# Performance work log

Measured on AMD Instinct MI355X. Metric: run time of the kernel, lower is better.

The kernel has to match this reference:

```python
import jax, jax.numpy as jnp
import numpy as np

NUM_HEADS = 32
HEAD_DIM = 128
NUM_KV_HEADS = 8
SCALE = 0.08838834764831845  # 1/sqrt(128)
SEQ_LEN = 2048
TOTAL_TOKENS = 4096  # batch=2 sequences of 2048


def setup_inputs() -> dict:
    key = jax.random.key(0)
    kq, kk, kv = jax.random.split(key, 3)
    q = jax.random.normal(kq, (TOTAL_TOKENS, NUM_HEADS * HEAD_DIM), dtype=jnp.float32)
    k = jax.random.normal(kk, (TOTAL_TOKENS, NUM_KV_HEADS * HEAD_DIM), dtype=jnp.float32)
    v = jax.random.normal(kv, (TOTAL_TOKENS, NUM_KV_HEADS * HEAD_DIM), dtype=jnp.float32)
    return {"q": q, "k": k, "v": v, "seq_len": SEQ_LEN}


def reference(q, k, v, seq_len):
    # Unified (varlen) causal GQA attention: flattened tokens are split into
    # batch sequences of equal length (the prefill path of the unified kernel).
    T = q.shape[0]
    B = T // seq_len
    G = NUM_HEADS // NUM_KV_HEADS  # query heads per kv head
    # [B, S, Hkv, G, D] and [B, S, Hkv, D]
    qh = q.reshape(B, seq_len, NUM_KV_HEADS, G, HEAD_DIM)
    kh = k.reshape(B, seq_len, NUM_KV_HEADS, HEAD_DIM)
    vh = v.reshape(B, seq_len, NUM_KV_HEADS, HEAD_DIM)
    # scores: [B, Hkv, G, Sq, Sk]
    scores = jnp.einsum("bqhgd,bkhd->bhgqk", qh, kh) * SCALE
    causal = jnp.tril(jnp.ones((seq_len, seq_len), dtype=bool))
    scores = jnp.where(causal, scores, jnp.finfo(scores.dtype).min)
    probs = jax.nn.softmax(scores, axis=-1)
    # out: [B, Sq, Hkv, G, D]
    o = jnp.einsum("bhgqk,bkhd->bqhgd", probs, vh)
    return o.reshape(T, NUM_HEADS * HEAD_DIM)
```

## Files before the change

### kernel.cpp

```cpp
#include <hip/hip_runtime.h>
#include <stdint.h>
#include <stddef.h>


#define S_LEN   2048
#define HQ      32
#define HKV     8
#define DH      128
#define QSTRIDE (HQ*DH)
#define KSTRIDE (HKV*DH)
#define SCALE_L2 0.12751139830213113f
#define DEFER_THR 8.0f

#define KTILE      64
#define NTILES     (S_LEN/KTILE)
#define CSTRIDE    520
#define KPART      (16*CSTRIDE)
#define TILE_ELEMS (KPART + 16*CSTRIDE)

typedef __bf16 bf16;
typedef short        s16x4 __attribute__((ext_vector_type(4)));
typedef short        s16x8 __attribute__((ext_vector_type(8)));
typedef float        f32x4 __attribute__((ext_vector_type(4)));
typedef unsigned int u32x2 __attribute__((ext_vector_type(2)));
typedef unsigned int u32x4 __attribute__((ext_vector_type(4)));

__device__ __forceinline__ unsigned int pk2(float a, float b) {
  union { bf16 h[2]; unsigned int u; } x;
  x.h[0] = (bf16)a; x.h[1] = (bf16)b;
  return x.u;
}

__device__ __forceinline__ int koff(int chunk, int key) {
  return chunk*CSTRIDE + key*8;
}
__device__ __forceinline__ int voff(int unit, int d) {
  return KPART + unit*CSTRIDE + d*4;
}

__global__ __launch_bounds__(512, 4)
void attn_fwd(const float* __restrict__ qg, const float* __restrict__ kg,
              const float* __restrict__ vg, float* __restrict__ og) {
  __shared__ bf16 smem[2*TILE_ELEMS];

  const int tid   = threadIdx.x;
  const int lane  = tid & 63;
  const int wave  = tid >> 6;
  const int l15   = lane & 15;
  const int quad  = lane >> 4;
  const int pairp = blockIdx.x;
  const int h     = blockIdx.y;
  const int b     = blockIdx.z;
  const int hkv   = h >> 2;

  const int fk_key = tid >> 3, fk_cg = tid & 7;
  const int fv_u   = tid & 15, fv_dq = tid >> 4;
  float4 fkx[4], fvx[4];

  auto load_regs = [&](int t) {
    const float* kp = kg + (size_t)(b*S_LEN + t*KTILE + fk_key)*KSTRIDE
                         + hkv*DH + fk_cg*16;
#pragma unroll
    for (int i = 0; i < 4; ++i) fkx[i] = ((const float4*)kp)[i];
    const int d0 = fv_dq*4;
#pragma unroll
    for (int j = 0; j < 4; ++j)
      fvx[j] = *(const float4*)(vg + (size_t)(b*S_LEN + t*KTILE + fv_u*4 + j)*KSTRIDE
                                   + hkv*DH + d0);
  };
  auto store_tile = [&](int bi) {
    bf16* kb = smem + bi*TILE_ELEMS;
#pragma unroll
    for (int ii = 0; ii < 2; ++ii) {
      u32x4 w;
      w[0] = pk2(fkx[2*ii].x,   fkx[2*ii].y);   w[1] = pk2(fkx[2*ii].z,   fkx[2*ii].w);
      w[2] = pk2(fkx[2*ii+1].x, fkx[2*ii+1].y); w[3] = pk2(fkx[2*ii+1].z, fkx[2*ii+1].w);
      *(u32x4*)(kb + koff(fk_cg*2 + ii, fk_key)) = w;
    }
    const float* g0 = (const float*)&fvx[0];
    const float* g1 = (const float*)&fvx[1];
    const float* g2 = (const float*)&fvx[2];
    const float* g3 = (const float*)&fvx[3];
#pragma unroll
    for (int i = 0; i < 4; i += 2) {
      u32x4 w;
      w[0] = pk2(g0[i],   g1[i]);
      w[1] = pk2(g2[i],   g3[i]);
      w[2] = pk2(g0[i+1], g1[i+1]);
      w[3] = pk2(g2[i+1], g3[i+1]);
      *(u32x4*)(kb + voff(fv_u, fv_dq*4 + i)) = w;
    }
  };

  f32x4 oacc[8];
  float m_run, l_run;
  u32x4 qf[4];

  const int qbs[2] = { pairp, 15 - pairp };
  load_regs(0);

  int gs = 0;
#pragma unroll 1
  for (int item = 0; item < 2; ++item) {
    const int qblk = qbs[item];
    const int qw   = qblk*128 + wave*16;
    const int nst  = qblk*2 + 2;

    {
      const float* qp = qg + (size_t)(b*S_LEN + qw + l15)*QSTRIDE
                           + h*DH + quad*8;
#pragma unroll
      for (int c = 0; c < 4; ++c) {
        const float4 a4 = ((const float4*)(qp + c*32))[0];
        const float4 b4 = ((const float4*)(qp + c*32))[1];
        u32x4 w;
        w[0] = pk2(a4.x*SCALE_L2, a4.y*SCALE_L2);
        w[1] = pk2(a4.z*SCALE_L2, a4.w*SCALE_L2);
        w[2] = pk2(b4.x*SCALE_L2, b4.y*SCALE_L2);
        w[3] = pk2(b4.z*SCALE_L2, b4.w*SCALE_L2);
        qf[c] = w;
      }
    }
#pragma unroll
    for (int nd = 0; nd < 8; ++nd) oacc[nd] = (f32x4){0.f, 0.f, 0.f, 0.f};
    m_run = -3e38f; l_run = 0.f;

#pragma unroll 1
    for (int i = 0; i < nst; ++i, ++gs) {
      const int k0  = i*KTILE;
      const int buf = gs & 1;
      store_tile(buf);
      const bool more  = (i + 1 < nst);
      const bool cross = (!more) && (item == 0);
      if (more)       load_regs(i + 1);
      else if (cross) load_regs(0);
      __syncthreads();

      if (k0 <= qw + 15) {
        const bf16* kb = smem + buf*TILE_ELEMS;

        f32x4 sacc[4];
#pragma unroll
        for (int mt = 0; mt < 4; ++mt) sacc[mt] = (f32x4){0.f, 0.f, 0.f, 0.f};
#pragma unroll
        for (int c = 0; c < 4; ++c) {
#pragma unroll
          for (int mt = 0; mt < 4; ++mt) {
            const u32x4 af = *(const u32x4*)(kb + koff(c*4 + quad, mt*16 + l15));
            sacc[mt] = __builtin_amdgcn_mfma_f32_16x16x32_bf16(
                __builtin_bit_cast(s16x8, af), __builtin_bit_cast(s16x8, qf[c]),
                sacc[mt], 0, 0, 0);
          }
        }

        const bool needmask = (k0 + KTILE - 1 > qw);
        const int  qgl = qw + l15;
        if (needmask) {
#pragma unroll
          for (int mt = 0; mt < 4; ++mt)
#pragma unroll
            for (int r = 0; r < 4; ++r) {
              const int key = k0 + mt*16 + quad*4 + r;
              if (key > qgl) sacc[mt][r] = -3e38f;
            }
        }
        float tmax;
        {
          float t8[8];
#pragma unroll
          for (int j = 0; j < 8; ++j)
            t8[j] = fmaxf(sacc[j >> 2][j & 3], sacc[(j >> 2) + 2][j & 3]);
          float t4[4];
#pragma unroll
          for (int j = 0; j < 4; ++j) t4[j] = fmaxf(t8[j], t8[j + 4]);
          tmax = fmaxf(fmaxf(t4[0], t4[2]), fmaxf(t4[1], t4[3]));
        }
        tmax = fmaxf(tmax, __shfl_xor(tmax, 16));
        tmax = fmaxf(tmax, __shfl_xor(tmax, 32));

        const bool defer = __all(tmax <= m_run + DEFER_THR);
        float alpha = 1.0f;
        if (!defer) {
          const float mnew = fmaxf(m_run, tmax);
          alpha = __builtin_amdgcn_exp2f(m_run - mnew);
          m_run = mnew;
        }
#pragma unroll
        for (int mt = 0; mt < 4; ++mt)
#pragma unroll
          for (int r = 0; r < 4; ++r)
            sacc[mt][r] = __builtin_amdgcn_exp2f(sacc[mt][r] - m_run);
        float rsum;
        {
          float s8[8];
#pragma unroll
          for (int j = 0; j < 8; ++j)
            s8[j] = sacc[j >> 2][j & 3] + sacc[(j >> 2) + 2][j & 3];
          float s4[4];
#pragma unroll
          for (int j = 0; j < 4; ++j) s4[j] = s8[j] + s8[j + 4];
          rsum = (s4[0] + s4[2]) + (s4[1] + s4[3]);
        }
        rsum += __shfl_xor(rsum, 16);
        rsum += __shfl_xor(rsum, 32);

        if (defer) {
          l_run += rsum;
        } else {
          l_run = l_run*alpha + rsum;
#pragma unroll
          for (int r = 0; r < 4; ++r) {
            const float a = __shfl(alpha, (lane & 48) | (quad*4 + r));
#pragma unroll
            for (int nd = 0; nd < 8; ++nd) oacc[nd][r] *= a;
          }
        }

        s16x4 pa[4];
#pragma unroll
        for (int mt = 0; mt < 4; ++mt) {
          union { bf16 hh[4]; s16x4 s; } u;
#pragma unroll
          for (int r = 0; r < 4; ++r) u.hh[r] = (bf16)sacc[mt][r];
          pa[mt] = u.s;
        }

#pragma unroll
        for (int kt = 0; kt < 4; ++kt)
#pragma unroll
          for (int nd = 0; nd < 8; ++nd) {
            const s16x4 bv = *(const s16x4*)(kb + voff(kt*4 + quad, nd*16 + l15));
            oacc[nd] = __builtin_amdgcn_mfma_f32_16x16x16bf16_1k(
                pa[kt], bv, oacc[nd], 0, 0, 0);
          }
      }
    }

#pragma unroll
    for (int r = 0; r < 4; ++r) {
      const float li  = __shfl(l_run, (lane & 48) | (quad*4 + r));
      const float inv = 1.0f / li;
      const size_t base = (size_t)(b*S_LEN + qw + quad*4 + r)*QSTRIDE
                        + h*DH + l15;
#pragma unroll
      for (int nd = 0; nd < 8; ++nd)
        og[base + nd*16] = oacc[nd][r] * inv;
    }
  }
}

extern "C" void kernel_launch(void* const* d_in, const int* in_sizes, int n_in,
                              void* d_out, int out_size, void* d_ws, size_t ws_size,
                              hipStream_t stream) {
  const float* q = (const float*)d_in[0];
  const float* k = (const float*)d_in[1];
  const float* v = (const float*)d_in[2];
  float* out = (float*)d_out;
  (void)d_ws; (void)ws_size;
  dim3 grid(8, HQ, 2);
  dim3 block(512);
  attn_fwd<<<grid, block, 0, stream>>>(q, k, v, out);
}
```

Baseline: 257.5 us.

## Process two 16-row query sub-blocks per wave with 256-thread blocks

Each wave now handles 32 query rows as two 16-row sub-tiles, so every K and V fragment read from LDS feeds two MFMAs. The block shrinks from 512 to 256 threads, and each thread now loads twice as much of every K/V tile. The aim is to halve LDS read traffic per unit of MFMA work and to improve instruction-level parallelism. In exchange, per-thread register use roughly doubles (two accumulator sets and two softmax states), which lowers occupancy and may cause spills.

```diff
diff --git a/kernel.cpp b/kernel.cpp
--- a/kernel.cpp
+++ b/kernel.cpp
@@ -22,7 +22,6 @@
 typedef short        s16x4 __attribute__((ext_vector_type(4)));
 typedef short        s16x8 __attribute__((ext_vector_type(8)));
 typedef float        f32x4 __attribute__((ext_vector_type(4)));
-typedef unsigned int u32x2 __attribute__((ext_vector_type(2)));
 typedef unsigned int u32x4 __attribute__((ext_vector_type(4)));
 
 __device__ __forceinline__ unsigned int pk2(float a, float b) {
@@ -38,7 +37,7 @@
   return KPART + unit*CSTRIDE + d*4;
 }
 
-__global__ __launch_bounds__(512, 4)
+__global__ __launch_bounds__(256, 2)
 void attn_fwd(const float* __restrict__ qg, const float* __restrict__ kg,
               const float* __restrict__ vg, float* __restrict__ og) {
   __shared__ bf16 smem[2*TILE_ELEMS];
@@ -53,48 +52,123 @@
   const int b     = blockIdx.z;
   const int hkv   = h >> 2;
 
-  const int fk_key = tid >> 3, fk_cg = tid & 7;
-  const int fv_u   = tid & 15, fv_dq = tid >> 4;
-  float4 fkx[4], fvx[4];
+  const int fk_key = tid >> 2, fk_cg = tid & 3;
+  const int fv_u   = tid & 15, fv_dg = tid >> 4;
+  float4 fkx[8], fvx[8];
 
   auto load_regs = [&](int t) {
     const float* kp = kg + (size_t)(b*S_LEN + t*KTILE + fk_key)*KSTRIDE
-                         + hkv*DH + fk_cg*16;
-#pragma unroll
-    for (int i = 0; i < 4; ++i) fkx[i] = ((const float4*)kp)[i];
-    const int d0 = fv_dq*4;
-#pragma unroll
-    for (int j = 0; j < 4; ++j)
-      fvx[j] = *(const float4*)(vg + (size_t)(b*S_LEN + t*KTILE + fv_u*4 + j)*KSTRIDE
-                                   + hkv*DH + d0);
+                         + hkv*DH + fk_cg*32;
+#pragma unroll
+    for (int i = 0; i < 8; ++i) fkx[i] = ((const float4*)kp)[i];
+    const int d0 = fv_dg*8;
+#pragma unroll
+    for (int r = 0; r < 4; ++r) {
+      const float* vp = vg + (size_t)(b*S_LEN + t*KTILE + fv_u*4 + r)*KSTRIDE
+                           + hkv*DH + d0;
+      fvx[2*r]   = ((const float4*)vp)[0];
+      fvx[2*r+1] = ((const float4*)vp)[1];
+    }
   };
   auto store_tile = [&](int bi) {
     bf16* kb = smem + bi*TILE_ELEMS;
 #pragma unroll
-    for (int ii = 0; ii < 2; ++ii) {
+    for (int j = 0; j < 4; ++j) {
       u32x4 w;
-      w[0] = pk2(fkx[2*ii].x,   fkx[2*ii].y);   w[1] = pk2(fkx[2*ii].z,   fkx[2*ii].w);
-      w[2] = pk2(fkx[2*ii+1].x, fkx[2*ii+1].y); w[3] = pk2(fkx[2*ii+1].z, fkx[2*ii+1].w);
-      *(u32x4*)(kb + koff(fk_cg*2 + ii, fk_key)) = w;
-    }
-    const float* g0 = (const float*)&fvx[0];
-    const float* g1 = (const float*)&fvx[1];
-    const float* g2 = (const float*)&fvx[2];
-    const float* g3 = (const float*)&fvx[3];
-#pragma unroll
-    for (int i = 0; i < 4; i += 2) {
+      w[0] = pk2(fkx[2*j].x,   fkx[2*j].y);   w[1] = pk2(fkx[2*j].z,   fkx[2*j].w);
+      w[2] = pk2(fkx[2*j+1].x, fkx[2*j+1].y); w[3] = pk2(fkx[2*j+1].z, fkx[2*j+1].w);
+      *(u32x4*)(kb + koff(fk_cg*4 + j, fk_key)) = w;
+    }
+    const float* F0 = (const float*)&fvx[0];
+    const float* F1 = (const float*)&fvx[2];
+    const float* F2 = (const float*)&fvx[4];
+    const float* F3 = (const float*)&fvx[6];
+#pragma unroll
+    for (int i = 0; i < 4; ++i) {
       u32x4 w;
-      w[0] = pk2(g0[i],   g1[i]);
-      w[1] = pk2(g2[i],   g3[i]);
-      w[2] = pk2(g0[i+1], g1[i+1]);
-      w[3] = pk2(g2[i+1], g3[i+1]);
-      *(u32x4*)(kb + voff(fv_u, fv_dq*4 + i)) = w;
+      w[0] = pk2(F0[2*i],   F1[2*i]);
+      w[1] = pk2(F2[2*i],   F3[2*i]);
+      w[2] = pk2(F0[2*i+1], F1[2*i+1]);
+      w[3] = pk2(F2[2*i+1], F3[2*i+1]);
+      *(u32x4*)(kb + voff(fv_u, fv_dg*8 + 2*i)) = w;
     }
   };
 
-  f32x4 oacc[8];
-  float m_run, l_run;
-  u32x4 qf[4];
+  auto softmax_sub = [&](int k0, int qsub, f32x4 (&sacc)[4], float& m_run,
+                         float& l_run, f32x4 (&oacc)[8], s16x4 (&pa)[4]) {
+    const int qgl = qsub + l15;
+    if (k0 + KTILE - 1 > qsub) {
+#pragma unroll
+      for (int mt = 0; mt < 4; ++mt)
+#pragma unroll
+        for (int r = 0; r < 4; ++r) {
+          const int key = k0 + mt*16 + quad*4 + r;
+          if (key > qgl) sacc[mt][r] = -3e38f;
+        }
+    }
+    float tmax;
+    {
+      float t8[8];
+#pragma unroll
+      for (int j = 0; j < 8; ++j)
+        t8[j] = fmaxf(sacc[j >> 2][j & 3], sacc[(j >> 2) + 2][j & 3]);
+      float t4[4];
+#pragma unroll
+      for (int j = 0; j < 4; ++j) t4[j] = fmaxf(t8[j], t8[j + 4]);
+      tmax = fmaxf(fmaxf(t4[0], t4[2]), fmaxf(t4[1], t4[3]));
+    }
+    tmax = fmaxf(tmax, __shfl_xor(tmax, 16));
+    tmax = fmaxf(tmax, __shfl_xor(tmax, 32));
+
+    const bool defer = __all(tmax <= m_run + DEFER_THR);
+    float alpha = 1.0f;
+    if (!defer) {
+      const float mnew = fmaxf(m_run, tmax);
+      alpha = __builtin_amdgcn_exp2f(m_run - mnew);
+      m_run = mnew;
+    }
+#pragma unroll
+    for (int mt = 0; mt < 4; ++mt)
+#pragma unroll
+      for (int r = 0; r < 4; ++r)
+        sacc[mt][r] = __builtin_amdgcn_exp2f(sacc[mt][r] - m_run);
+    float rsum;
+    {
+      float s8[8];
+#pragma unroll
+      for (int j = 0; j < 8; ++j)
+        s8[j] = sacc[j >> 2][j & 3] + sacc[(j >> 2) + 2][j & 3];
+      float s4[4];
+#pragma unroll
+      for (int j = 0; j < 4; ++j) s4[j] = s8[j] + s8[j + 4];
+      rsum = (s4[0] + s4[2]) + (s4[1] + s4[3]);
+    }
+    rsum += __shfl_xor(rsum, 16);
+    rsum += __shfl_xor(rsum, 32);
+
+    if (defer) {
+      l_run += rsum;
+    } else {
+      l_run = l_run*alpha + rsum;
+#pragma unroll
+      for (int r = 0; r < 4; ++r) {
+        const float a = __shfl(alpha, (lane & 48) | (quad*4 + r));
+#pragma unroll
+        for (int nd = 0; nd < 8; ++nd) oacc[nd][r] *= a;
+      }
+    }
+#pragma unroll
+    for (int mt = 0; mt < 4; ++mt) {
+      union { bf16 hh[4]; s16x4 s; } u;
+#pragma unroll
+      for (int r = 0; r < 4; ++r) u.hh[r] = (bf16)sacc[mt][r];
+      pa[mt] = u.s;
+    }
+  };
+
+  f32x4 oacc0[8], oacc1[8];
+  float m0, l0, m1, l1;
+  u32x4 qf0[4], qf1[4];
 
   const int qbs[2] = { pairp, 15 - pairp };
   load_regs(0);
@@ -103,27 +177,44 @@
 #pragma unroll 1
   for (int item = 0; item < 2; ++item) {
     const int qblk = qbs[item];
-    const int qw   = qblk*128 + wave*16;
+    const int qw   = qblk*128 + wave*32;
     const int nst  = qblk*2 + 2;
 
     {
-      const float* qp = qg + (size_t)(b*S_LEN + qw + l15)*QSTRIDE
-                           + h*DH + quad*8;
+      const float* qp0 = qg + (size_t)(b*S_LEN + qw + l15)*QSTRIDE
+                            + h*DH + quad*8;
+      const float* qp1 = qp0 + (size_t)16*QSTRIDE;
 #pragma unroll
       for (int c = 0; c < 4; ++c) {
-        const float4 a4 = ((const float4*)(qp + c*32))[0];
-        const float4 b4 = ((const float4*)(qp + c*32))[1];
-        u32x4 w;
-        w[0] = pk2(a4.x*SCALE_L2, a4.y*SCALE_L2);
-        w[1] = pk2(a4.z*SCALE_L2, a4.w*SCALE_L2);
-        w[2] = pk2(b4.x*SCALE_L2, b4.y*SCALE_L2);
-        w[3] = pk2(b4.z*SCALE_L2, b4.w*SCALE_L2);
-        qf[c] = w;
+        {
+          const float4 a4 = ((const float4*)(qp0 + c*32))[0];
+          const float4 b4 = ((const float4*)(qp0 + c*32))[1];
+          u32x4 w;
+          w[0] = pk2(a4.x*SCALE_L2, a4.y*SCALE_L2);
+          w[1] = pk2(a4.z*SCALE_L2, a4.w*SCALE_L2);
+          w[2] = pk2(b4.x*SCALE_L2, b4.y*SCALE_L2);
+          w[3] = pk2(b4.z*SCALE_L2, b4.w*SCALE_L2);
+          qf0[c] = w;
+        }
+        {
+          const float4 a4 = ((const float4*)(qp1 + c*32))[0];
+          const float4 b4 = ((const float4*)(qp1 + c*32))[1];
+          u32x4 w;
+          w[0] = pk2(a4.x*SCALE_L2, a4.y*SCALE_L2);
+          w[1] = pk2(a4.z*SCALE_L2, a4.w*SCALE_L2);
+          w[2] = pk2(b4.x*SCALE_L2, b4.y*SCALE_L2);
+          w[3] = pk2(b4.z*SCALE_L2, b4.w*SCALE_L2);
+          qf1[c] = w;
+        }
       }
     }
 #pragma unroll
-    for (int nd = 0; nd < 8; ++nd) oacc[nd] = (f32x4){0.f, 0.f, 0.f, 0.f};
-    m_run = -3e38f; l_run = 0.f;
+    for (int nd = 0; nd < 8; ++nd) {
+      oacc0[nd] = (f32x4){0.f, 0.f, 0.f, 0.f};
+      oacc1[nd] = (f32x4){0.f, 0.f, 0.f, 0.f};
+    }
+    m0 = -3e38f; l0 = 0.f;
+    m1 = -3e38f; l1 = 0.f;
 
 #pragma unroll 1
     for (int i = 0; i < nst; ++i, ++gs) {
@@ -136,115 +227,63 @@
       else if (cross) load_regs(0);
       __syncthreads();
 
-      if (k0 <= qw + 15) {
+      if (k0 <= qw + 31) {
         const bf16* kb = smem + buf*TILE_ELEMS;
 
-        f32x4 sacc[4];
-#pragma unroll
-        for (int mt = 0; mt < 4; ++mt) sacc[mt] = (f32x4){0.f, 0.f, 0.f, 0.f};
+        f32x4 sacc0[4], sacc1[4];
+#pragma unroll
+        for (int mt = 0; mt < 4; ++mt) {
+          sacc0[mt] = (f32x4){0.f, 0.f, 0.f, 0.f};
+          sacc1[mt] = (f32x4){0.f, 0.f, 0.f, 0.f};
+        }
 #pragma unroll
         for (int c = 0; c < 4; ++c) {
 #pragma unroll
           for (int mt = 0; mt < 4; ++mt) {
             const u32x4 af = *(const u32x4*)(kb + koff(c*4 + quad, mt*16 + l15));
-            sacc[mt] = __builtin_amdgcn_mfma_f32_16x16x32_bf16(
-                __builtin_bit_cast(s16x8, af), __builtin_bit_cast(s16x8, qf[c]),
-                sacc[mt], 0, 0, 0);
+            sacc0[mt] = __builtin_amdgcn_mfma_f32_16x16x32_bf16(
+                __builtin_bit_cast(s16x8, af), __builtin_bit_cast(s16x8, qf0[c]),
+                sacc0[mt], 0, 0, 0);
+            sacc1[mt] = __builtin_amdgcn_mfma_f32_16x16x32_bf16(
+                __builtin_bit_cast(s16x8, af), __builtin_bit_cast(s16x8, qf1[c]),
+                sacc1[mt], 0, 0, 0);
           }
         }
 
-        const bool needmask = (k0 + KTILE - 1 > qw);
-        const int  qgl = qw + l15;
-        if (needmask) {
-#pragma unroll
-          for (int mt = 0; mt < 4; ++mt)
-#pragma unroll
-            for (int r = 0; r < 4; ++r) {
-              const int key = k0 + mt*16 + quad*4 + r;
-              if (key > qgl) sacc[mt][r] = -3e38f;
-            }
-        }
-        float tmax;
-        {
-          float t8[8];
-#pragma unroll
-          for (int j = 0; j < 8; ++j)
-            t8[j] = fmaxf(sacc[j >> 2][j & 3], sacc[(j >> 2) + 2][j & 3]);
-          float t4[4];
-#pragma unroll
-          for (int j = 0; j < 4; ++j) t4[j] = fmaxf(t8[j], t8[j + 4]);
-          tmax = fmaxf(fmaxf(t4[0], t4[2]), fmaxf(t4[1], t4[3]));
-        }
-        tmax = fmaxf(tmax, __shfl_xor(tmax, 16));
-        tmax = fmaxf(tmax, __shfl_xor(tmax, 32));
-
-        const bool defer = __all(tmax <= m_run + DEFER_THR);
-        float alpha = 1.0f;
-        if (!defer) {
-          const float mnew = fmaxf(m_run, tmax);
-          alpha = __builtin_amdgcn_exp2f(m_run - mnew);
-          m_run = mnew;
-        }
-#pragma unroll
-        for (int mt = 0; mt < 4; ++mt)
-#pragma unroll
-          for (int r = 0; r < 4; ++r)
-            sacc[mt][r] = __builtin_amdgcn_exp2f(sacc[mt][r] - m_run);
-        float rsum;
-        {
-          float s8[8];
-#pragma unroll
-          for (int j = 0; j < 8; ++j)
-            s8[j] = sacc[j >> 2][j & 3] + sacc[(j >> 2) + 2][j & 3];
-          float s4[4];
-#pragma unroll
-          for (int j = 0; j < 4; ++j) s4[j] = s8[j] + s8[j + 4];
-          rsum = (s4[0] + s4[2]) + (s4[1] + s4[3]);
-        }
-        rsum += __shfl_xor(rsum, 16);
-        rsum += __shfl_xor(rsum, 32);
-
-        if (defer) {
-          l_run += rsum;
-        } else {
-          l_run = l_run*alpha + rsum;
-#pragma unroll
-          for (int r = 0; r < 4; ++r) {
-            const float a = __shfl(alpha, (lane & 48) | (quad*4 + r));
-#pragma unroll
-            for (int nd = 0; nd < 8; ++nd) oacc[nd][r] *= a;
-          }
-        }
-
-        s16x4 pa[4];
-#pragma unroll
-        for (int mt = 0; mt < 4; ++mt) {
-          union { bf16 hh[4]; s16x4 s; } u;
-#pragma unroll
-          for (int r = 0; r < 4; ++r) u.hh[r] = (bf16)sacc[mt][r];
-          pa[mt] = u.s;
-        }
+        s16x4 pa0[4], pa1[4];
+        softmax_sub(k0, qw,      sacc0, m0, l0, oacc0, pa0);
+        softmax_sub(k0, qw + 16, sacc1, m1, l1, oacc1, pa1);
 
 #pragma unroll
         for (int kt = 0; kt < 4; ++kt)
 #pragma unroll
           for (int nd = 0; nd < 8; ++nd) {
             const s16x4 bv = *(const s16x4*)(kb + voff(kt*4 + quad, nd*16 + l15));
-            oacc[nd] = __builtin_amdgcn_mfma_f32_16x16x16bf16_1k(
-                pa[kt], bv, oacc[nd], 0, 0, 0);
+            oacc0[nd] = __builtin_amdgcn_mfma_f32_16x16x16bf16_1k(
+                pa0[kt], bv, oacc0[nd], 0, 0, 0);
+            oacc1[nd] = __builtin_amdgcn_mfma_f32_16x16x16bf16_1k(
+                pa1[kt], bv, oacc1[nd], 0, 0, 0);
           }
       }
     }
 
 #pragma unroll
     for (int r = 0; r < 4; ++r) {
-      const float li  = __shfl(l_run, (lane & 48) | (quad*4 + r));
-      const float inv = 1.0f / li;
-      const size_t base = (size_t)(b*S_LEN + qw + quad*4 + r)*QSTRIDE
-                        + h*DH + l15;
+      const float li0 = __shfl(l0, (lane & 48) | (quad*4 + r));
+      const float inv0 = 1.0f / li0;
+      const size_t base0 = (size_t)(b*S_LEN + qw + quad*4 + r)*QSTRIDE
+                         + h*DH + l15;
 #pragma unroll
       for (int nd = 0; nd < 8; ++nd)
-        og[base + nd*16] = oacc[nd][r] * inv;
+        og[base0 + nd*16] = oacc0[nd][r] * inv0;
+
+      const float li1 = __shfl(l1, (lane & 48) | (quad*4 + r));
+      const float inv1 = 1.0f / li1;
+      const size_t base1 = (size_t)(b*S_LEN + qw + 16 + quad*4 + r)*QSTRIDE
+                         + h*DH + l15;
+#pragma unroll
+      for (int nd = 0; nd < 8; ++nd)
+        og[base1 + nd*16] = oacc1[nd][r] * inv1;
     }
   }
 }
@@ -258,6 +297,6 @@
   float* out = (float*)d_out;
   (void)d_ws; (void)ws_size;
   dim3 grid(8, HQ, 2);
-  dim3 block(512);
+  dim3 block(256);
   attn_fwd<<<grid, block, 0, stream>>>(q, k, v, out);
 }
```

Result: slower. 287.4 us (+11.6%).
